# Performance work log

Hardware: AMD Instinct MI355X
Metric: run time of the kernel (lower is better)

## Reference

```python
import jax, jax.numpy as jnp
import numpy as np

N_POST_NMS = 2000      # Config.train_n_nms
MIN_SIZE = 16.0        # Config.prop_min_size
IMG_H = 800.0          # Config.input_shape[0]
IMG_W = 800.0          # Config.input_shape[1]
NMS_THRESH = 0.7       # Config.nms_thresh
N_PROPOSALS = 8192


def setup_inputs() -> dict:
    key = jax.random.key(0)
    k1, k2, k3 = jax.random.split(key, 3)
    # bbox_locs rows are (cy, cx, h, w); make them plausible for an 800x800 image
    ctr = jax.random.uniform(k1, (N_PROPOSALS, 2), dtype=jnp.float32) * 800.0
    sz = jax.random.uniform(k2, (N_PROPOSALS, 2), dtype=jnp.float32) * 260.0 + 4.0
    bbox_locs = jnp.concatenate([ctr, sz], axis=1)
    object_scores = jax.random.uniform(k3, (N_PROPOSALS,), dtype=jnp.float32)
    return {"bbox_locs": bbox_locs, "object_scores": object_scores}


def _decode_clip(bbox_locs):
    # center/size -> corners (y1,x1,y2,x2), size filter BEFORE clipping (as in source)
    cy, cx, h, w = bbox_locs[:, 0], bbox_locs[:, 1], bbox_locs[:, 2], bbox_locs[:, 3]
    y1, x1 = cy - 0.5 * h, cx - 0.5 * w
    y2, x2 = cy + 0.5 * h, cx + 0.5 * w
    valid = ((y2 - y1) > MIN_SIZE) & ((x2 - x1) > MIN_SIZE)
    boxes = jnp.stack([
        jnp.clip(y1, 0.0, IMG_H),
        jnp.clip(x1, 0.0, IMG_W),
        jnp.clip(y2, 0.0, IMG_H),
        jnp.clip(x2, 0.0, IMG_W),
    ], axis=1)  # [N,4]
    return boxes, valid


def _iou_matrix(b):
    # pairwise IoU, same convention as tf.image.non_max_suppression (no +1)
    y1, x1, y2, x2 = b[:, 0], b[:, 1], b[:, 2], b[:, 3]
    area = (y2 - y1) * (x2 - x1)
    iy = jnp.maximum(0.0, jnp.minimum(y2[:, None], y2[None, :]) - jnp.maximum(y1[:, None], y1[None, :]))
    ix = jnp.maximum(0.0, jnp.minimum(x2[:, None], x2[None, :]) - jnp.maximum(x1[:, None], x1[None, :]))
    inter = iy * ix
    union = area[:, None] + area[None, :] - inter
    return jnp.where(union > 0.0, inter / union, 0.0)


def _nms_select(boxes, scores, valid):
    # Greedy NMS. Invalid (too-small) boxes get -inf score so they sort last and
    # start suppressed -- equivalent to the tf.gather filtering in the original.
    N = boxes.shape[0]
    order = jnp.argsort(-jnp.where(valid, scores, -jnp.inf))
    bs = boxes[order]
    iou = _iou_matrix(bs)  # [N,N]
    idx = jnp.arange(N)

    def body(i, state):
        suppressed, kept = state
        keep_i = jnp.logical_not(suppressed[i])
        kept = kept.at[i].set(keep_i)
        suppressed = suppressed | (keep_i & (iou[i] > NMS_THRESH) & (idx > i))
        return suppressed, kept

    suppressed0 = jnp.logical_not(valid[order])
    kept0 = jnp.zeros((N,), dtype=bool)
    _, kept = jax.lax.fori_loop(0, N, body, (suppressed0, kept0))

    # first N_POST_NMS kept boxes in score order (same as max_output_size in TF)
    sel = jnp.nonzero(kept, size=N_POST_NMS, fill_value=0)[0]
    out_valid = jnp.arange(N_POST_NMS) < jnp.sum(kept)
    return order[sel], out_valid


def reference(bbox_locs, object_scores):
    boxes, valid = _decode_clip(bbox_locs)
    sel_idx, out_valid = _nms_select(boxes, object_scores, valid)
    # pad slots beyond the number of kept boxes with zeros (fixed output shape)
    return jnp.where(out_valid[:, None], boxes[sel_idx], 0.0)
```

## Files before the change

### kernel.cpp

```cpp
#include <hip/hip_runtime.h>
#include <cstdint>
#include <cstddef>

typedef unsigned long long ull;
typedef unsigned short u16;

#define N 8192
#define NWORDS 128
#define NPOST 2000
#define NMS_THR 0.7f
#define MASKW 48
#define SCAP 128
#define ICAP 16
#define NUNITS 312
#define SLICE_STRIDE 260


__device__ __forceinline__ float4 decode_clip_box(const float4 L, bool* valid) {
#pragma clang fp contract(off)
  float cy = L.x, cx = L.y, h = L.z, w = L.w;
  float y1 = cy - 0.5f * h;
  float x1 = cx - 0.5f * w;
  float y2 = cy + 0.5f * h;
  float x2 = cx + 0.5f * w;
  *valid = ((y2 - y1) > 16.0f) && ((x2 - x1) > 16.0f);
  float4 b;
  b.x = fminf(fmaxf(y1, 0.0f), 800.0f);
  b.y = fminf(fmaxf(x1, 0.0f), 800.0f);
  b.z = fminf(fmaxf(y2, 0.0f), 800.0f);
  b.w = fminf(fmaxf(x2, 0.0f), 800.0f);
  return b;
}

__device__ __forceinline__ float box_area(const float4 b) {
#pragma clang fp contract(off)
  return (b.z - b.x) * (b.w - b.y);
}

__device__ __forceinline__ bool iou_gt_thr(const float4 a, float aa,
                                           const float4 b, float ab) {
#pragma clang fp contract(off)
  float iy = fminf(a.z, b.z) - fmaxf(a.x, b.x);
  float ix = fminf(a.w, b.w) - fmaxf(a.y, b.y);
  iy = fmaxf(iy, 0.0f);
  ix = fmaxf(ix, 0.0f);
  float inter = iy * ix;
  float uni = aa + ab - inter;
  return (inter > 0.0f) && (uni > 0.0f) && ((inter / uni) > NMS_THR);
}

__device__ __forceinline__ ull resolve_word(ull dg, ull avail, int lane) {
  ull conflict = __ballot(((dg & avail) != 0ull) && ((avail >> lane) & 1ull));
  if (conflict == 0ull) return avail;
  ull dgT = 0ull;
  #pragma unroll
  for (int c = 0; c < 64; ++c) {
    ull tb = __ballot((dg >> c) & 1ull);
    if (lane == c) dgT = tb;
  }
  ull kept = avail;
  while (true) {
    bool sup = (dgT & kept) != 0ull;
    ull kn = avail & ~__ballot(sup);
    if (kn == kept) break;
    kept = kn;
  }
  return kept;
}

__global__ __launch_bounds__(256) void rankgather_kernel(
    const float* __restrict__ locs, const float* __restrict__ scores,
    float4* __restrict__ bs, float* __restrict__ area,
    int* __restrict__ ctrl, int* __restrict__ inCnt) {
  __shared__ float ssc[32 * SLICE_STRIDE];
  __shared__ int sRank[8][33];
  int tid = threadIdx.x, bid = blockIdx.x;
  if (bid == 0) {
    if (tid < 64) ctrl[tid] = 0;
    else if (tid < 128) inCnt[tid - 64] = 0;
  }
  const float4* locs4 = (const float4*)locs;
  for (int k = 0; k < 32; ++k) {
    int j = k * 256 + tid;
    bool v; (void)decode_clip_box(locs4[j], &v);
    float s = v ? scores[j] : -__builtin_inff();
    ssc[(j >> 8) * SLICE_STRIDE + (j & 255)] = s;
  }
  __syncthreads();
  int boxOff = tid & 7;
  int part = tid >> 3;
  int i = bid * 8 + boxOff;
  float si = ssc[(i >> 8) * SLICE_STRIDE + (i & 255)];
  const float4* s4 = (const float4*)(ssc + part * SLICE_STRIDE);
  int j0 = part * 256;
  int cnt = 0;
  for (int q = 0; q < 64; ++q) {
    float4 v = s4[q];
    int j = j0 + 4 * q;
    cnt += (v.x > si) || ((v.x == si) & ((j + 0) < i));
    cnt += (v.y > si) || ((v.y == si) & ((j + 1) < i));
    cnt += (v.z > si) || ((v.z == si) & ((j + 2) < i));
    cnt += (v.w > si) || ((v.w == si) & ((j + 3) < i));
  }
  sRank[boxOff][part] = cnt;
  __syncthreads();
  if (tid < 8) {
    int r = 0;
    #pragma unroll
    for (int p = 0; p < 32; ++p) r += sRank[tid][p];
    int ig = bid * 8 + tid;
    bool v;
    float4 b = decode_clip_box(locs4[ig], &v);
    bs[r] = b;
    area[r] = v ? box_area(b) : -1.0f;
  }
}

__global__ __launch_bounds__(256) void pairs_kernel(
    const float4* __restrict__ bs, const float* __restrict__ area,
    int* __restrict__ ctrl, int* __restrict__ inCnt,
    unsigned* __restrict__ srcBuf, unsigned* __restrict__ inBuf) {
  __shared__ float4 sb[4][64];
  __shared__ float  sa[4][64];
  int tid = threadIdx.x;
  int u = blockIdx.x;
  int cbq = 0;
  while (2 * (cbq + 1) * (cbq + 2) <= u) ++cbq;
  int rb = u - 2 * cbq * (cbq + 1);
  int lane = tid & 63, cq = tid >> 6;
  int cb = cbq * 4 + cq;
  int j0 = cb * 64;
  sb[cq][lane] = bs[j0 + lane];
  sa[cq][lane] = area[j0 + lane];
  int i = rb * 64 + lane;
  float4 r = bs[i];
  float ai = area[i];
  __syncthreads();
  if (cb < rb || ai < 0.0f) return;
  ull bits = 0;
  for (int c = 0; c < 64; ++c) {
    if ((j0 + c) > i && sa[cq][c] >= 0.0f &&
        iou_gt_thr(r, ai, sb[cq][c], sa[cq][c]))
      bits |= 1ull << c;
  }
  int n = (int)__popcll(bits);
  if (!n) return;
  if (cb == rb) {
    int base = atomicAdd(&inCnt[cb], n);
    if (base + n > ICAP) { ctrl[48] = 1; return; }
    int k = base;
    while (bits) {
      int c = (int)__builtin_ctzll(bits); bits &= bits - 1;
      inBuf[cb * ICAP + k++] = ((unsigned)c << 8) | (unsigned)lane;
    }
  } else {
    int base = atomicAdd(&ctrl[rb], n);
    if (base + n > SCAP) { ctrl[48] = 1; return; }
    int k = base;
    while (bits) {
      int c = (int)__builtin_ctzll(bits); bits &= bits - 1;
      srcBuf[rb * SCAP + k++] =
          ((unsigned)lane << 13) | ((unsigned)cb << 6) | (unsigned)c;
    }
  }
}

__global__ __launch_bounds__(256) void scan_kernel(
    const float4* __restrict__ bs, const float* __restrict__ area,
    const int* __restrict__ ctrl, const int* __restrict__ inCnt,
    const unsigned* __restrict__ srcBuf, const unsigned* __restrict__ inBuf,
    float* __restrict__ out) {
  __shared__ __align__(16) char smem[35840];
  int tid = threadIdx.x;

  unsigned (*sSrc)[SCAP] = (unsigned(*)[SCAP])(smem + 0);
  unsigned (*sIn)[ICAP]  = (unsigned(*)[ICAP])(smem + 24576);
  int*  sSCnt     = (int*)(smem + 27648);
  int*  sICnt     = (int*)(smem + 27840);
  ull*  sRemv     = (ull*)(smem + 28032);
  u16*  sKeptList = (u16*)(smem + 29056);
  float4* sWB     = (float4*)(smem + 33056);
  float*  sWA     = (float*)(smem + 34080);
  ull*  sSupW     = (ull*)(smem + 34336);
  int*  sCtl      = (int*)(smem + 34344);

  {
    int wave = tid >> 6, lane = tid & 63;
    for (int b = 0; b < 4; ++b) {
      float av[8];
      #pragma unroll
      for (int q = 0; q < 8; ++q)
        av[q] = area[(wave + (b * 8 + q) * 4) * 64 + lane];
      #pragma unroll
      for (int q = 0; q < 8; ++q) {
        ull inv = __ballot(av[q] < 0.0f);
        if (lane == 0) sRemv[wave + (b * 8 + q) * 4] = inv;
      }
    }
  }
  if (tid == 254) sCtl[0] = 0;
  if (tid == 253) sCtl[1] = 0;
  if (tid < MASKW) { sSCnt[tid] = ctrl[tid]; sICnt[tid] = inCnt[tid]; }
  if (tid == 255) sCtl[2] = ctrl[48];
  {
    const uint4* src4 = (const uint4*)srcBuf;
    uint4* dst4 = (uint4*)sSrc;
    #pragma unroll
    for (int k = 0; k < 6; ++k) dst4[tid + k * 256] = src4[tid + k * 256];
    const uint4* in4 = (const uint4*)inBuf;
    if (tid < 192) ((uint4*)sIn)[tid] = in4[tid];
  }
  __syncthreads();

  int sOver = sCtl[2];
  if (!sOver && tid < 64) {
    int lane = tid;
    int base = 0;
    for (int w = 0; w < MASKW; ++w) {
      ull avail = ~sRemv[w];
      int cnI = sICnt[w];
      ull kept;
      if (cnI == 0) {
        kept = avail;
      } else {
        ull dgT = 0ull;
        for (int k = 0; k < cnI; ++k) {
          unsigned p = sIn[w][k];
          int il = (int)(p & 63u);
          int jl = (int)(p >> 8) & 63;
          if (lane == jl) dgT |= 1ull << il;
        }
        ull cf = __ballot(((dgT & avail) != 0ull) && ((avail >> lane) & 1ull));
        if (cf == 0ull) {
          kept = avail;
        } else {
          kept = avail;
          while (true) {
            bool sup = (dgT & kept) != 0ull;
            ull kn = avail & ~__ballot(sup);
            if (kn == kept) break;
            kept = kn;
          }
        }
      }
      if ((kept >> lane) & 1ull) {
        int rank = base + (int)__popcll(kept & ((1ull << lane) - 1ull));
        if (rank < NPOST) sKeptList[rank] = (u16)(w * 64 + lane);
      }
      base += (int)__popcll(kept);
      if (base >= NPOST) break;
      int cnS = sSCnt[w];
      for (int k = lane; k < cnS; k += 64) {
        unsigned p = sSrc[w][k];
        int il = (int)(p >> 13) & 63;
        if ((kept >> il) & 1ull) {
          int wt = (int)(p >> 6) & 127;
          atomicOr(&sRemv[wt], 1ull << (p & 63u));
        }
      }
    }
    if (lane == 0) { sCtl[0] = base; if (base >= NPOST) sCtl[1] = 1; }
  }
  __syncthreads();

  int startW = sOver ? 0 : MASKW;
  if (!sCtl[1]) {
    for (int w = startW; w < NWORDS; ++w) {
      if (tid < 64) { sWB[tid] = bs[w * 64 + tid]; sWA[tid] = area[w * 64 + tid]; }
      if (tid == 0) *sSupW = sRemv[w];
      __syncthreads();
      int nk = sCtl[0];
      int c = tid & 63;
      for (int k0 = tid >> 6; k0 < nk; k0 += 4) {
        int ki = sKeptList[k0];
        float4 kb = bs[ki];
        bool s = iou_gt_thr(kb, area[ki], sWB[c], sWA[c]);
        ull bits = __ballot(s);
        if (c == 0 && bits) atomicOr(sSupW, bits);
      }
      __syncthreads();
      if (tid < 64) {
        int lane = tid;
        float4 bm = sWB[lane];
        float am = sWA[lane];
        ull dg = 0;
        if (am >= 0.0f) {
          for (int cc = lane + 1; cc < 64; ++cc)
            if (sWA[cc] >= 0.0f && iou_gt_thr(bm, am, sWB[cc], sWA[cc]))
              dg |= 1ull << cc;
        }
        ull avail = ~*sSupW;
        ull kept = resolve_word(dg, avail, lane);
        int base = sCtl[0];
        if ((kept >> lane) & 1ull) {
          int rank = base + (int)__popcll(kept & ((1ull << lane) - 1ull));
          if (rank < NPOST) sKeptList[rank] = (u16)(w * 64 + lane);
        }
        if (lane == 0) {
          int nb = base + (int)__popcll(kept);
          sCtl[0] = nb;
          if (nb >= NPOST) sCtl[1] = 1;
        }
      }
      __syncthreads();
      if (sCtl[1]) break;
    }
  }

  __syncthreads();
  int total = sCtl[0];
  if (total > NPOST) total = NPOST;
  for (int r = tid; r < NPOST; r += 256) {
    float4 v = make_float4(0.0f, 0.0f, 0.0f, 0.0f);
    if (r < total) v = bs[sKeptList[r]];
    reinterpret_cast<float4*>(out)[r] = v;
  }
  if (total == 0 && tid == 0)
    out[0] = 5.0e9f + (float)sCtl[2] * 1.0e8f;
}

extern "C" void kernel_launch(void* const* d_in, const int* in_sizes, int n_in,
                              void* d_out, int out_size, void* d_ws, size_t ws_size,
                              hipStream_t stream) {
  const float* locs   = (const float*)d_in[0];
  const float* scores = (const float*)d_in[1];

  char* ws = (char*)d_ws;
  float4*   bs       = (float4*)(ws + 0);
  float*    area     = (float*)(ws + 131072);
  int*      ctrl     = (int*)(ws + 163840);
  int*      inCnt    = (int*)(ws + 164096);
  unsigned* srcBuf   = (unsigned*)(ws + 164352);
  unsigned* inBuf    = (unsigned*)(ws + 188928);

  rankgather_kernel<<<N / 8, 256, 0, stream>>>(locs, scores, bs, area, ctrl, inCnt);
  pairs_kernel<<<NUNITS, 256, 0, stream>>>(bs, area, ctrl, inCnt, srcBuf, inBuf);
  scan_kernel<<<1, 256, 0, stream>>>(bs, area, ctrl, inCnt, srcBuf, inBuf,
                                     (float*)d_out);
}
```

Measured before the change: 60.94 us.

## Fuse rank and pair-IoU kernels by computing pairs in original index space

Merges the rank/gather kernel and the pairwise IoU kernel into one launch. The pair blocks now decode boxes directly from the input in original index order over all 8192 boxes, and write candidate pairs per unit into fixed-capacity buffers. The single-block scan kernel maps those pairs to sorted ranks through a new rankOf table and bins them into its shared-memory lists. This removes a launch and the dependency on the sorted box order, but it runs many more pair blocks over the full N instead of only the top 48 words, and it adds serial remapping work to the single-block scan.

```diff
diff --git a/kernel.cpp b/kernel.cpp
--- a/kernel.cpp
+++ b/kernel.cpp
@@ -12,7 +12,9 @@
 #define MASKW 48
 #define SCAP 128
 #define ICAP 16
-#define NUNITS 312
+#define NUNITS_P 2112
+#define RANKB 1024
+#define UCAP 24
 #define SLICE_STRIDE 260
 
 
@@ -68,18 +70,67 @@
   return kept;
 }
 
-__global__ __launch_bounds__(256) void rankgather_kernel(
+__global__ __launch_bounds__(256) void rankpairs_kernel(
     const float* __restrict__ locs, const float* __restrict__ scores,
-    float4* __restrict__ bs, float* __restrict__ area,
-    int* __restrict__ ctrl, int* __restrict__ inCnt) {
-  __shared__ float ssc[32 * SLICE_STRIDE];
-  __shared__ int sRank[8][33];
+    float4* __restrict__ bs, float* __restrict__ area, u16* __restrict__ rankOf,
+    unsigned char* __restrict__ cntU, unsigned* __restrict__ pairBuf) {
+  __shared__ __align__(16) char smem[34336];
   int tid = threadIdx.x, bid = blockIdx.x;
-  if (bid == 0) {
-    if (tid < 64) ctrl[tid] = 0;
-    else if (tid < 128) inCnt[tid - 64] = 0;
-  }
   const float4* locs4 = (const float4*)locs;
+
+  if (bid < NUNITS_P) {
+    float4* sb = (float4*)smem;
+    float*  sa = (float*)(smem + 4096);
+    int* sCnt  = (int*)(smem + 5120);
+    int* sOver = (int*)(smem + 5124);
+    if (tid == 0) { *sCnt = 0; *sOver = 0; }
+    int u = bid;
+    int cbq = 0;
+    while (2 * (cbq + 1) * (cbq + 2) <= u) ++cbq;
+    int rb = u - 2 * cbq * (cbq + 1);
+    int lane = tid & 63, cq = tid >> 6;
+    int cbO = cbq * 4 + cq;
+    int j0 = cbO * 64;
+    bool vC;
+    float4 cbx = decode_clip_box(locs4[j0 + lane], &vC);
+    sb[cq * 64 + lane] = cbx;
+    sa[cq * 64 + lane] = vC ? box_area(cbx) : -1.0f;
+    int i = rb * 64 + lane;
+    bool vR;
+    float4 r = decode_clip_box(locs4[i], &vR);
+    float ai = vR ? box_area(r) : -1.0f;
+    __syncthreads();
+    if (cbO >= rb && ai >= 0.0f) {
+      ull bits = 0;
+      for (int c = 0; c < 64; ++c) {
+        if ((j0 + c) > i && sa[cq * 64 + c] >= 0.0f &&
+            iou_gt_thr(r, ai, sb[cq * 64 + c], sa[cq * 64 + c]))
+          bits |= 1ull << c;
+      }
+      int n = (int)__popcll(bits);
+      if (n) {
+        int base = atomicAdd(sCnt, n);
+        int k = base;
+        while (bits) {
+          int c = (int)__builtin_ctzll(bits); bits &= bits - 1;
+          if (k < UCAP) pairBuf[u * UCAP + k] = ((unsigned)i << 13) |
+                                                (unsigned)(j0 + c);
+          else *sOver = 1;
+          ++k;
+        }
+      }
+    }
+    __syncthreads();
+    if (tid == 0) {
+      int c = *sCnt;
+      cntU[u] = (unsigned char)(*sOver ? 255 : (c > UCAP ? 255 : c));
+    }
+    return;
+  }
+
+  float* ssc = (float*)smem;
+  int (*sRank)[33] = (int(*)[33])(smem + 33280);
+  int brid = bid - NUNITS_P;
   for (int k = 0; k < 32; ++k) {
     int j = k * 256 + tid;
     bool v; (void)decode_clip_box(locs4[j], &v);
@@ -89,7 +140,7 @@
   __syncthreads();
   int boxOff = tid & 7;
   int part = tid >> 3;
-  int i = bid * 8 + boxOff;
+  int i = brid * 8 + boxOff;
   float si = ssc[(i >> 8) * SLICE_STRIDE + (i & 255)];
   const float4* s4 = (const float4*)(ssc + part * SLICE_STRIDE);
   int j0 = part * 256;
@@ -108,68 +159,19 @@
     int r = 0;
     #pragma unroll
     for (int p = 0; p < 32; ++p) r += sRank[tid][p];
-    int ig = bid * 8 + tid;
+    int ig = brid * 8 + tid;
     bool v;
     float4 b = decode_clip_box(locs4[ig], &v);
     bs[r] = b;
     area[r] = v ? box_area(b) : -1.0f;
-  }
-}
-
-__global__ __launch_bounds__(256) void pairs_kernel(
-    const float4* __restrict__ bs, const float* __restrict__ area,
-    int* __restrict__ ctrl, int* __restrict__ inCnt,
-    unsigned* __restrict__ srcBuf, unsigned* __restrict__ inBuf) {
-  __shared__ float4 sb[4][64];
-  __shared__ float  sa[4][64];
-  int tid = threadIdx.x;
-  int u = blockIdx.x;
-  int cbq = 0;
-  while (2 * (cbq + 1) * (cbq + 2) <= u) ++cbq;
-  int rb = u - 2 * cbq * (cbq + 1);
-  int lane = tid & 63, cq = tid >> 6;
-  int cb = cbq * 4 + cq;
-  int j0 = cb * 64;
-  sb[cq][lane] = bs[j0 + lane];
-  sa[cq][lane] = area[j0 + lane];
-  int i = rb * 64 + lane;
-  float4 r = bs[i];
-  float ai = area[i];
-  __syncthreads();
-  if (cb < rb || ai < 0.0f) return;
-  ull bits = 0;
-  for (int c = 0; c < 64; ++c) {
-    if ((j0 + c) > i && sa[cq][c] >= 0.0f &&
-        iou_gt_thr(r, ai, sb[cq][c], sa[cq][c]))
-      bits |= 1ull << c;
-  }
-  int n = (int)__popcll(bits);
-  if (!n) return;
-  if (cb == rb) {
-    int base = atomicAdd(&inCnt[cb], n);
-    if (base + n > ICAP) { ctrl[48] = 1; return; }
-    int k = base;
-    while (bits) {
-      int c = (int)__builtin_ctzll(bits); bits &= bits - 1;
-      inBuf[cb * ICAP + k++] = ((unsigned)c << 8) | (unsigned)lane;
-    }
-  } else {
-    int base = atomicAdd(&ctrl[rb], n);
-    if (base + n > SCAP) { ctrl[48] = 1; return; }
-    int k = base;
-    while (bits) {
-      int c = (int)__builtin_ctzll(bits); bits &= bits - 1;
-      srcBuf[rb * SCAP + k++] =
-          ((unsigned)lane << 13) | ((unsigned)cb << 6) | (unsigned)c;
-    }
+    rankOf[ig] = (u16)r;
   }
 }
 
 __global__ __launch_bounds__(256) void scan_kernel(
     const float4* __restrict__ bs, const float* __restrict__ area,
-    const int* __restrict__ ctrl, const int* __restrict__ inCnt,
-    const unsigned* __restrict__ srcBuf, const unsigned* __restrict__ inBuf,
-    float* __restrict__ out) {
+    const u16* __restrict__ rankOf, const unsigned char* __restrict__ cntU,
+    const unsigned* __restrict__ pairBuf, float* __restrict__ out) {
   __shared__ __align__(16) char smem[35840];
   int tid = threadIdx.x;
 
@@ -183,6 +185,12 @@
   float*  sWA     = (float*)(smem + 34080);
   ull*  sSupW     = (ull*)(smem + 34336);
   int*  sCtl      = (int*)(smem + 34344);
+
+  if (tid < MASKW) { sSCnt[tid] = 0; sICnt[tid] = 0; }
+  if (tid == 254) sCtl[0] = 0;
+  if (tid == 253) sCtl[1] = 0;
+  if (tid == 252) sCtl[2] = 0;
+  __syncthreads();
 
   {
     int wave = tid >> 6, lane = tid & 63;
@@ -198,17 +206,31 @@
       }
     }
   }
-  if (tid == 254) sCtl[0] = 0;
-  if (tid == 253) sCtl[1] = 0;
-  if (tid < MASKW) { sSCnt[tid] = ctrl[tid]; sICnt[tid] = inCnt[tid]; }
-  if (tid == 255) sCtl[2] = ctrl[48];
-  {
-    const uint4* src4 = (const uint4*)srcBuf;
-    uint4* dst4 = (uint4*)sSrc;
-    #pragma unroll
-    for (int k = 0; k < 6; ++k) dst4[tid + k * 256] = src4[tid + k * 256];
-    const uint4* in4 = (const uint4*)inBuf;
-    if (tid < 192) ((uint4*)sIn)[tid] = in4[tid];
+
+  for (int u = tid; u < NUNITS_P; u += 256) {
+    int c = cntU[u];
+    if (c == 255) { sCtl[2] = 1; continue; }
+    for (int k = 0; k < c; ++k) {
+      unsigned p = pairBuf[u * UCAP + k];
+      int a = (int)(p >> 13), b2 = (int)(p & 8191u);
+      int ra = rankOf[a], rb2 = rankOf[b2];
+      int lo = ra < rb2 ? ra : rb2;
+      int hi = ra < rb2 ? rb2 : ra;
+      if (hi >= MASKW * 64) continue;
+      int wlo = lo >> 6, whi = hi >> 6;
+      if (wlo == whi) {
+        int slot = atomicAdd(&sICnt[wlo], 1);
+        if (slot < ICAP)
+          sIn[wlo][slot] = ((unsigned)(hi & 63) << 8) | (unsigned)(lo & 63);
+        else sCtl[2] = 1;
+      } else {
+        int slot = atomicAdd(&sSCnt[wlo], 1);
+        if (slot < SCAP)
+          sSrc[wlo][slot] = ((unsigned)(lo & 63) << 13) |
+                            ((unsigned)whi << 6) | (unsigned)(hi & 63);
+        else sCtl[2] = 1;
+      }
+    }
   }
   __syncthreads();
 
@@ -326,15 +348,14 @@
   const float* scores = (const float*)d_in[1];
 
   char* ws = (char*)d_ws;
-  float4*   bs       = (float4*)(ws + 0);
-  float*    area     = (float*)(ws + 131072);
-  int*      ctrl     = (int*)(ws + 163840);
-  int*      inCnt    = (int*)(ws + 164096);
-  unsigned* srcBuf   = (unsigned*)(ws + 164352);
-  unsigned* inBuf    = (unsigned*)(ws + 188928);
-
-  rankgather_kernel<<<N / 8, 256, 0, stream>>>(locs, scores, bs, area, ctrl, inCnt);
-  pairs_kernel<<<NUNITS, 256, 0, stream>>>(bs, area, ctrl, inCnt, srcBuf, inBuf);
-  scan_kernel<<<1, 256, 0, stream>>>(bs, area, ctrl, inCnt, srcBuf, inBuf,
+  float4*        bs      = (float4*)(ws + 0);
+  float*         area    = (float*)(ws + 131072);
+  u16*           rankOf  = (u16*)(ws + 163840);
+  unsigned char* cntU    = (unsigned char*)(ws + 180224);
+  unsigned*      pairBuf = (unsigned*)(ws + 184320);
+
+  rankpairs_kernel<<<NUNITS_P + RANKB, 256, 0, stream>>>(
+      locs, scores, bs, area, rankOf, cntU, pairBuf);
+  scan_kernel<<<1, 256, 0, stream>>>(bs, area, rankOf, cntU, pairBuf,
                                      (float*)d_out);
 }
```

Result: slower. 111.6 us (+83.1%).

## Replace sequential per-word NMS scan with parallel fixed-point iteration over target buckets

Applied to the files above, without the earlier changes.

Suppression pairs are now grouped by target word into a single bucket array, instead of being split into separate source and intra-word buffers. The single-block scan no longer walks the 48 words one after another. Instead, 48 lanes, one per word, iterate Jacobi-style: each lane recomputes its kept mask from the current global kept masks until no mask changes. A prefix sum over per-word counts then builds the kept list. This removes the serial word-by-word dependency chain. In exchange, the number of iterations depends on the depth of the suppression chains, and each iteration rescans every bucket.

```diff
diff --git a/kernel.cpp b/kernel.cpp
--- a/kernel.cpp
+++ b/kernel.cpp
@@ -10,8 +10,7 @@
 #define NPOST 2000
 #define NMS_THR 0.7f
 #define MASKW 48
-#define SCAP 128
-#define ICAP 16
+#define TCAP 160
 #define NUNITS 312
 #define SLICE_STRIDE 260
 
@@ -70,15 +69,11 @@
 
 __global__ __launch_bounds__(256) void rankgather_kernel(
     const float* __restrict__ locs, const float* __restrict__ scores,
-    float4* __restrict__ bs, float* __restrict__ area,
-    int* __restrict__ ctrl, int* __restrict__ inCnt) {
+    float4* __restrict__ bs, float* __restrict__ area, int* __restrict__ ctrl) {
   __shared__ float ssc[32 * SLICE_STRIDE];
   __shared__ int sRank[8][33];
   int tid = threadIdx.x, bid = blockIdx.x;
-  if (bid == 0) {
-    if (tid < 64) ctrl[tid] = 0;
-    else if (tid < 128) inCnt[tid - 64] = 0;
-  }
+  if (bid == 0 && tid < 64) ctrl[tid] = 0;
   const float4* locs4 = (const float4*)locs;
   for (int k = 0; k < 32; ++k) {
     int j = k * 256 + tid;
@@ -118,8 +113,7 @@
 
 __global__ __launch_bounds__(256) void pairs_kernel(
     const float4* __restrict__ bs, const float* __restrict__ area,
-    int* __restrict__ ctrl, int* __restrict__ inCnt,
-    unsigned* __restrict__ srcBuf, unsigned* __restrict__ inBuf) {
+    int* __restrict__ ctrl, unsigned* __restrict__ buck) {
   __shared__ float4 sb[4][64];
   __shared__ float  sa[4][64];
   int tid = threadIdx.x;
@@ -145,44 +139,31 @@
   }
   int n = (int)__popcll(bits);
   if (!n) return;
-  if (cb == rb) {
-    int base = atomicAdd(&inCnt[cb], n);
-    if (base + n > ICAP) { ctrl[48] = 1; return; }
-    int k = base;
-    while (bits) {
-      int c = (int)__builtin_ctzll(bits); bits &= bits - 1;
-      inBuf[cb * ICAP + k++] = ((unsigned)c << 8) | (unsigned)lane;
-    }
-  } else {
-    int base = atomicAdd(&ctrl[rb], n);
-    if (base + n > SCAP) { ctrl[48] = 1; return; }
-    int k = base;
-    while (bits) {
-      int c = (int)__builtin_ctzll(bits); bits &= bits - 1;
-      srcBuf[rb * SCAP + k++] =
-          ((unsigned)lane << 13) | ((unsigned)cb << 6) | (unsigned)c;
-    }
+  int base = atomicAdd(&ctrl[cb], n);
+  if (base + n > TCAP) { ctrl[48] = 1; return; }
+  int k = base;
+  while (bits) {
+    int c = (int)__builtin_ctzll(bits); bits &= bits - 1;
+    buck[cb * TCAP + k++] = ((unsigned)c << 13) | (unsigned)i;
   }
 }
 
 __global__ __launch_bounds__(256) void scan_kernel(
     const float4* __restrict__ bs, const float* __restrict__ area,
-    const int* __restrict__ ctrl, const int* __restrict__ inCnt,
-    const unsigned* __restrict__ srcBuf, const unsigned* __restrict__ inBuf,
+    const int* __restrict__ ctrl, const unsigned* __restrict__ buck,
     float* __restrict__ out) {
-  __shared__ __align__(16) char smem[35840];
+  __shared__ __align__(16) char smem[37760];
   int tid = threadIdx.x;
 
-  unsigned (*sSrc)[SCAP] = (unsigned(*)[SCAP])(smem + 0);
-  unsigned (*sIn)[ICAP]  = (unsigned(*)[ICAP])(smem + 24576);
-  int*  sSCnt     = (int*)(smem + 27648);
-  int*  sICnt     = (int*)(smem + 27840);
-  ull*  sRemv     = (ull*)(smem + 28032);
-  u16*  sKeptList = (u16*)(smem + 29056);
-  float4* sWB     = (float4*)(smem + 33056);
-  float*  sWA     = (float*)(smem + 34080);
-  ull*  sSupW     = (ull*)(smem + 34336);
-  int*  sCtl      = (int*)(smem + 34344);
+  unsigned (*sBuck)[TCAP] = (unsigned(*)[TCAP])(smem + 0);
+  int*  sCnt      = (int*)(smem + 30720);
+  ull*  sRemv     = (ull*)(smem + 30912);
+  ull*  sKept     = (ull*)(smem + 31936);
+  u16*  sKeptList = (u16*)(smem + 32448);
+  float4* sWB     = (float4*)(smem + 36448);
+  float*  sWA     = (float*)(smem + 37472);
+  ull*  sSupW     = (ull*)(smem + 37728);
+  int*  sCtl      = (int*)(smem + 37736);
 
   {
     int wave = tid >> 6, lane = tid & 63;
@@ -200,66 +181,58 @@
   }
   if (tid == 254) sCtl[0] = 0;
   if (tid == 253) sCtl[1] = 0;
-  if (tid < MASKW) { sSCnt[tid] = ctrl[tid]; sICnt[tid] = inCnt[tid]; }
+  if (tid < MASKW) sCnt[tid] = ctrl[tid];
   if (tid == 255) sCtl[2] = ctrl[48];
   {
-    const uint4* src4 = (const uint4*)srcBuf;
-    uint4* dst4 = (uint4*)sSrc;
+    const uint4* b4 = (const uint4*)buck;
+    uint4* d4 = (uint4*)sBuck;
     #pragma unroll
-    for (int k = 0; k < 6; ++k) dst4[tid + k * 256] = src4[tid + k * 256];
-    const uint4* in4 = (const uint4*)inBuf;
-    if (tid < 192) ((uint4*)sIn)[tid] = in4[tid];
+    for (int k = 0; k < 8; ++k) {
+      int idx = tid + k * 256;
+      if (idx < (MASKW * TCAP) / 4) d4[idx] = b4[idx];
+    }
   }
   __syncthreads();
 
   int sOver = sCtl[2];
   if (!sOver && tid < 64) {
-    int lane = tid;
-    int base = 0;
-    for (int w = 0; w < MASKW; ++w) {
-      ull avail = ~sRemv[w];
-      int cnI = sICnt[w];
-      ull kept;
-      if (cnI == 0) {
-        kept = avail;
-      } else {
-        ull dgT = 0ull;
-        for (int k = 0; k < cnI; ++k) {
-          unsigned p = sIn[w][k];
-          int il = (int)(p & 63u);
-          int jl = (int)(p >> 8) & 63;
-          if (lane == jl) dgT |= 1ull << il;
-        }
-        ull cf = __ballot(((dgT & avail) != 0ull) && ((avail >> lane) & 1ull));
-        if (cf == 0ull) {
-          kept = avail;
-        } else {
-          kept = avail;
-          while (true) {
-            bool sup = (dgT & kept) != 0ull;
-            ull kn = avail & ~__ballot(sup);
-            if (kn == kept) break;
-            kept = kn;
-          }
-        }
+    int w = tid;
+    ull validw = (w < MASKW) ? ~sRemv[w] : 0ull;
+    int cw = (w < MASKW) ? sCnt[w] : 0;
+    if (cw > TCAP) cw = TCAP;
+    ull kept = validw;
+    for (int it = 0; it < 3072; ++it) {
+      sKept[w] = kept;
+      ull sup = 0;
+      for (int k = 0; k < cw; ++k) {
+        unsigned e = sBuck[w][k];
+        int sr = (int)(e & 8191u);
+        if ((sKept[sr >> 6] >> (sr & 63)) & 1ull) sup |= 1ull << (e >> 13);
       }
-      if ((kept >> lane) & 1ull) {
-        int rank = base + (int)__popcll(kept & ((1ull << lane) - 1ull));
-        if (rank < NPOST) sKeptList[rank] = (u16)(w * 64 + lane);
-      }
-      base += (int)__popcll(kept);
-      if (base >= NPOST) break;
-      int cnS = sSCnt[w];
-      for (int k = lane; k < cnS; k += 64) {
-        unsigned p = sSrc[w][k];
-        int il = (int)(p >> 13) & 63;
-        if ((kept >> il) & 1ull) {
-          int wt = (int)(p >> 6) & 127;
-          atomicOr(&sRemv[wt], 1ull << (p & 63u));
-        }
-      }
-    }
-    if (lane == 0) { sCtl[0] = base; if (base >= NPOST) sCtl[1] = 1; }
+      ull kn = validw & ~sup;
+      ull chg = __ballot(kn != kept);
+      kept = kn;
+      if (chg == 0ull) break;
+    }
+    sKept[w] = kept;
+    int cnt_w = (int)__popcll(kept);
+    int inc = cnt_w;
+    #pragma unroll
+    for (int d = 1; d < 64; d <<= 1) {
+      int t = __shfl_up(inc, d, 64);
+      if (w >= d) inc += t;
+    }
+    int idx = inc - cnt_w;
+    ull kb = kept;
+    while (kb) {
+      int b = (int)__builtin_ctzll(kb); kb &= kb - 1;
+      if (idx < NPOST) sKeptList[idx] = (u16)(w * 64 + b);
+      ++idx;
+    }
+    if (w == 63) {
+      sCtl[0] = inc;
+      if (inc >= NPOST) sCtl[1] = 1;
+    }
   }
   __syncthreads();
 
@@ -326,15 +299,12 @@
   const float* scores = (const float*)d_in[1];
 
   char* ws = (char*)d_ws;
-  float4*   bs       = (float4*)(ws + 0);
-  float*    area     = (float*)(ws + 131072);
-  int*      ctrl     = (int*)(ws + 163840);
-  int*      inCnt    = (int*)(ws + 164096);
-  unsigned* srcBuf   = (unsigned*)(ws + 164352);
-  unsigned* inBuf    = (unsigned*)(ws + 188928);
-
-  rankgather_kernel<<<N / 8, 256, 0, stream>>>(locs, scores, bs, area, ctrl, inCnt);
-  pairs_kernel<<<NUNITS, 256, 0, stream>>>(bs, area, ctrl, inCnt, srcBuf, inBuf);
-  scan_kernel<<<1, 256, 0, stream>>>(bs, area, ctrl, inCnt, srcBuf, inBuf,
-                                     (float*)d_out);
-}
+  float4*   bs   = (float4*)(ws + 0);
+  float*    area = (float*)(ws + 131072);
+  int*      ctrl = (int*)(ws + 163840);
+  unsigned* buck = (unsigned*)(ws + 164352);
+
+  rankgather_kernel<<<N / 8, 256, 0, stream>>>(locs, scores, bs, area, ctrl);
+  pairs_kernel<<<NUNITS, 256, 0, stream>>>(bs, area, ctrl, buck);
+  scan_kernel<<<1, 256, 0, stream>>>(bs, area, ctrl, buck, (float*)d_out);
+}
```

After: 71.23 us. 1.17x slower.
